# Optimization experiments

Hardware: AMD Instinct MI355X
Metric: run time of the kernel (lower is better)

The kernel has to match this reference:

```python
import jax, jax.numpy as jnp
import numpy as np

B, S, D = 1, 2048, 2048
H = 16            # num query heads
QL = 1536         # q_lora_rank
KVL = 512         # kv_lora_rank
DN = 128          # qk_nope_head_dim
DR = 64           # qk_rope_head_dim
DV = 128          # v_head_dim
F = 8192          # ffn intermediate
EPS = 1e-6
WAVE = 10000.0


def _rms(x, scale, eps=EPS):
    # fp32 norm then cast back, matching DeepSeekV3_1RMSNorm
    x32 = x.astype(jnp.float32)
    ms = jnp.mean(x32 * x32, axis=-1, keepdims=True)
    return (x32 * jax.lax.rsqrt(ms + eps)).astype(x.dtype) * scale


def _rope_tables(seq_len, dim):
    inv_freq = 1.0 / (WAVE ** (jnp.arange(0, dim, 2, dtype=jnp.float32) / dim))
    t = jnp.arange(seq_len, dtype=jnp.float32)[:, None] * inv_freq[None, :]  # [S, dim/2]
    emb = jnp.concatenate([t, t], axis=-1)  # [S, dim]
    return jnp.cos(emb), jnp.sin(emb)


def _apply_rope(x, cos, sin):
    # x: [B, S, H, dr]; rotate-half convention
    half = x.shape[-1] // 2
    x1, x2 = x[..., :half], x[..., half:]
    rot = jnp.concatenate([-x2, x1], axis=-1)
    return x * cos[None, :, None, :] + rot * sin[None, :, None, :]


def setup_inputs() -> dict:
    key = jax.random.key(0)
    ks = jax.random.split(key, 12)
    w = lambda k, shp: (jax.random.normal(k, shp, dtype=jnp.float32) * 0.02)
    inp = {
        "hidden_states": jax.random.normal(ks[0], (B, S, D), dtype=jnp.float32),
        "attention_mask": jnp.broadcast_to(jnp.tril(jnp.ones((S, S), dtype=bool)), (B, S, S)),
        "pre_attn_scale": jnp.ones((D,), jnp.float32),
        "wqa": w(ks[1], (D, QL)),
        "q_norm_scale": jnp.ones((QL,), jnp.float32),
        "wqb": w(ks[2], (QL, H * (DN + DR))),
        "wkva": w(ks[3], (D, KVL + DR)),
        "kv_norm_scale": jnp.ones((KVL,), jnp.float32),
        "wkvb": w(ks[4], (KVL, H * (DN + DV))),
        "wo": w(ks[5], (H * DV, D)),
        "pre_ffn_scale": jnp.ones((D,), jnp.float32),
        "wg": w(ks[6], (D, F)),
        "bg": jnp.zeros((F,), jnp.float32),
        "wu": w(ks[7], (D, F)),
        "bu": jnp.zeros((F,), jnp.float32),
        "wd": w(ks[8], (F, D)),
        "bd": jnp.zeros((D,), jnp.float32),
    }
    return inp


def reference(hidden_states, attention_mask, pre_attn_scale, wqa, q_norm_scale, wqb,
              wkva, kv_norm_scale, wkvb, wo, pre_ffn_scale, wg, bg, wu, bu, wd, bd):
    x = hidden_states
    # --- pre-attention RMSNorm ---
    n = _rms(x, pre_attn_scale)
    # --- MLA attention ---
    q = (_rms(n @ wqa, q_norm_scale) @ wqb).reshape(B, S, H, DN + DR)
    q_nope, q_rope = q[..., :DN], q[..., DN:]
    kva = n @ wkva                              # [B,S,KVL+DR]
    c_kv, k_rope = kva[..., :KVL], kva[..., KVL:]
    kv = (_rms(c_kv, kv_norm_scale) @ wkvb).reshape(B, S, H, DN + DV)
    k_nope, v = kv[..., :DN], kv[..., DN:]
    cos, sin = _rope_tables(S, DR)
    q_rope = _apply_rope(q_rope, cos, sin)
    k_rope = _apply_rope(k_rope[:, :, None, :], cos, sin)  # [B,S,1,DR] shared across heads
    qf = jnp.concatenate([q_nope, q_rope], axis=-1)
    kf = jnp.concatenate([k_nope, jnp.broadcast_to(k_rope, (B, S, H, DR))], axis=-1)
    scale = 1.0 / float(np.sqrt(DN + DR))
    scores = jnp.einsum('bqhd,bkhd->bhqk', qf, kf) * scale
    scores = jnp.where(attention_mask[:, None, :, :], scores, jnp.float32(-1e9))
    probs = jax.nn.softmax(scores, axis=-1)
    attn = jnp.einsum('bhqk,bkhd->bqhd', probs, v).reshape(B, S, H * DV)
    x = x + attn @ wo                            # residual 1 (dropout=0)
    # --- pre-FFN RMSNorm + dense SwiGLU FFN ---
    n = _rms(x, pre_ffn_scale)
    ff = (jax.nn.silu(n @ wg + bg) * (n @ wu + bu)) @ wd + bd
    return x + ff                                # residual 2
```

## Files before the change

kernel.cpp:

```cpp
#include <hip/hip_runtime.h>
#include <hip/hip_bf16.h>
#include <stdint.h>

typedef unsigned short u16;
using f32x4  = __attribute__((ext_vector_type(4))) float;
using bf16x8 = __attribute__((ext_vector_type(8))) __bf16;
using u32x4  = __attribute__((ext_vector_type(4))) uint32_t;
using u16x4  = __attribute__((ext_vector_type(4))) unsigned short;
using u16x8  = __attribute__((ext_vector_type(8))) unsigned short;

#define S_LEN 2048
#define DM    2048
#define NH    16
#define QLR   1536
#define KVLR  512
#define DNOPE 128
#define DROPE 64
#define DVAL  128
#define FFD   8192

static __device__ __forceinline__ float bf2f(u16 u) {
    union { uint32_t i; float f; } v; v.i = ((uint32_t)u) << 16; return v.f;
}
static __device__ __forceinline__ u16 f2bf(float f) {
    union { float f; uint32_t i; } v; v.f = f;
    uint32_t x = v.i;
    return (u16)((x + 0x7FFF + ((x >> 16) & 1)) >> 16);
}
static __device__ __forceinline__ void gload16(const u16* g, const u16* l) {
    __builtin_amdgcn_global_load_lds(
        (const __attribute__((address_space(1))) void*)g,
        (__attribute__((address_space(3))) void*)l, 16, 0, 0);
}

struct TWJob { const float* src; u16* dst; int R, C, xt, start; };
struct TWJobs { TWJob j[4]; };

__global__ __launch_bounds__(256)
void transpose_all(TWJobs jobs)
{
    __shared__ __align__(16) u16 tile[64][68];
    const int bid = blockIdx.x;
    int e = 0;
#pragma unroll
    for (int i = 1; i < 4; ++i) e = (bid >= jobs.j[i].start) ? i : e;
    const float* src = jobs.j[e].src;
    u16* dst = jobs.j[e].dst;
    const int R = jobs.j[e].R, C = jobs.j[e].C;
    const int local = bid - jobs.j[e].start;
    const int c0 = (local % jobs.j[e].xt) * 64;
    const int r0 = (local / jobs.j[e].xt) * 64;
    const int t = threadIdx.x;
#pragma unroll
    for (int i = 0; i < 4; ++i) {
        int idx = i * 256 + t;
        int r = idx >> 4, c4 = idx & 15;
        float4 v = *reinterpret_cast<const float4*>(&src[(size_t)(r0 + r) * C + c0 + c4 * 4]);
        u16x4 b; b[0] = f2bf(v.x); b[1] = f2bf(v.y); b[2] = f2bf(v.z); b[3] = f2bf(v.w);
        *reinterpret_cast<u16x4*>(&tile[r][c4 * 4]) = b;
    }
    __syncthreads();
#pragma unroll
    for (int i = 0; i < 4; ++i) {
        int idx = i * 256 + t;
        int rr = idx >> 4, k4 = idx & 15;
        u16x4 o;
#pragma unroll
        for (int j = 0; j < 4; ++j) o[j] = tile[k4 * 4 + j][rr];
        *reinterpret_cast<u16x4*>(&dst[(size_t)(c0 + rr) * R + r0 + k4 * 4]) = o;
    }
}

template<bool IN_F32>
__global__ __launch_bounds__(256)
void rms_norm(const void* __restrict__ in, int in_stride, int width,
              const float* __restrict__ scale, u16* __restrict__ out, int out_stride)
{
    const int row = blockIdx.x;
    const int t = threadIdx.x;
    const float* inf = (const float*)in;
    const u16*   inb = (const u16*)in;
    float ss = 0.f;
    for (int c = t; c < width; c += 256) {
        float v = IN_F32 ? inf[(size_t)row * in_stride + c] : bf2f(inb[(size_t)row * in_stride + c]);
        ss += v * v;
    }
#pragma unroll
    for (int o = 32; o > 0; o >>= 1) ss += __shfl_xor(ss, o);
    __shared__ float red[4];
    if ((t & 63) == 0) red[t >> 6] = ss;
    __syncthreads();
    float inv = rsqrtf((red[0] + red[1] + red[2] + red[3]) / (float)width + 1e-6f);
    for (int c = t; c < width; c += 256) {
        float v = IN_F32 ? inf[(size_t)row * in_stride + c] : bf2f(inb[(size_t)row * in_stride + c]);
        out[(size_t)row * out_stride + c] = f2bf(v * inv * scale[c]);
    }
}

__global__ __launch_bounds__(256)
void rms_norm2(const float* __restrict__ inA, int strideA, int widthA,
               const float* __restrict__ scaleA, u16* __restrict__ outA, int ostrA,
               const float* __restrict__ inB, int strideB, int widthB,
               const float* __restrict__ scaleB, u16* __restrict__ outB, int ostrB)
{
    const float* in   = blockIdx.y ? inB : inA;
    const float* scale= blockIdx.y ? scaleB : scaleA;
    u16* out          = blockIdx.y ? outB : outA;
    const int stride  = blockIdx.y ? strideB : strideA;
    const int width   = blockIdx.y ? widthB : widthA;
    const int ostr    = blockIdx.y ? ostrB : ostrA;
    const int row = blockIdx.x;
    const int t = threadIdx.x;
    float ss = 0.f;
    for (int c = t; c < width; c += 256) {
        float v = in[(size_t)row * stride + c];
        ss += v * v;
    }
#pragma unroll
    for (int o = 32; o > 0; o >>= 1) ss += __shfl_xor(ss, o);
    __shared__ float red[4];
    if ((t & 63) == 0) red[t >> 6] = ss;
    __syncthreads();
    float inv = rsqrtf((red[0] + red[1] + red[2] + red[3]) / (float)width + 1e-6f);
    for (int c = t; c < width; c += 256) {
        float v = in[(size_t)row * stride + c];
        out[(size_t)row * ostr + c] = f2bf(v * inv * scale[c]);
    }
}

__global__ __launch_bounds__(256)
void rope_tv(u16* __restrict__ q, const float* __restrict__ kva, u16* __restrict__ kr,
             const u16* __restrict__ kv, u16* __restrict__ vt)
{
    const int bid = blockIdx.x;
    const int t = threadIdx.x;
    if (bid < S_LEN) {
        const int s = bid;
        for (int idx = t; idx < 544; idx += 256) {
            int d = idx & 31;
            float invf = powf(10000.f, -(float)(2 * d) / 64.f);
            float ang = (float)s * invf;
            float cs = cosf(ang), sn = sinf(ang);
            if (idx < 512) {
                int hh = idx >> 5;
                u16* base = q + ((size_t)s * NH + hh) * 192 + 128;
                float x1 = bf2f(base[d]), x2 = bf2f(base[d + 32]);
                base[d]      = f2bf(x1 * cs - x2 * sn);
                base[d + 32] = f2bf(x2 * cs + x1 * sn);
            } else {
                const float* kb = kva + (size_t)s * 576 + 512;
                float x1 = kb[d], x2 = kb[d + 32];
                kr[(size_t)s * 64 + d]      = f2bf(x1 * cs - x2 * sn);
                kr[(size_t)s * 64 + d + 32] = f2bf(x2 * cs + x1 * sn);
            }
        }
        return;
    }
    __shared__ __align__(16) u16 tile[64][76];
    const int t2 = bid - S_LEN;
    const int s0 = (t2 & 31) * 64;
    const int d0 = ((t2 >> 5) & 1) * 64;
    const int h  = t2 >> 6;
#pragma unroll
    for (int i = 0; i < 2; ++i) {
        int idx = i * 256 + t;
        int s = idx >> 3, c8 = idx & 7;
        u16x8 v = *reinterpret_cast<const u16x8*>(kv + (size_t)(s0 + s) * (NH * 256) + h * 256 + 128 + d0 + c8 * 8);
        u16x4 lo, hi;
#pragma unroll
        for (int j = 0; j < 4; ++j) { lo[j] = v[j]; hi[j] = v[4 + j]; }
        *reinterpret_cast<u16x4*>(&tile[s][c8 * 8])     = lo;
        *reinterpret_cast<u16x4*>(&tile[s][c8 * 8 + 4]) = hi;
    }
    __syncthreads();
#pragma unroll
    for (int i = 0; i < 4; ++i) {
        int idx = i * 256 + t;
        int d = idx >> 4, s4 = idx & 15;
        u16x4 o;
#pragma unroll
        for (int j = 0; j < 4; ++j) o[j] = tile[s4 * 4 + j][d];
        *reinterpret_cast<u16x4*>(&vt[(size_t)(h * 128 + d0 + d) * S_LEN + s0 + s4 * 4]) = o;
    }
}

__global__ __launch_bounds__(256)
void init_out(const float* __restrict__ x2, const float* __restrict__ bd,
              float* __restrict__ out, int total4, int N)
{
    int i = blockIdx.x * 256 + threadIdx.x;
    const int stride = gridDim.x * 256;
    for (; i < total4; i += stride) {
        float4 r = ((const float4*)x2)[i];
        int col = (i * 4) & (N - 1);
        float4 b = *reinterpret_cast<const float4*>(&bd[col]);
        float4 o; o.x = r.x + b.x; o.y = r.y + b.y; o.z = r.z + b.z; o.w = r.w + b.w;
        ((float4*)out)[i] = o;
    }
}

__global__ __launch_bounds__(256)
void mul_gu(const u16* __restrict__ g, const u16* __restrict__ u,
            u16* __restrict__ h, int total8)
{
    int i = blockIdx.x * 256 + threadIdx.x;
    const int stride = gridDim.x * 256;
    for (; i < total8; i += stride) {
        u16x8 gv = ((const u16x8*)g)[i];
        u16x8 uv = ((const u16x8*)u)[i];
        u16x8 hv;
#pragma unroll
        for (int j = 0; j < 8; ++j) hv[j] = f2bf(bf2f(gv[j]) * bf2f(uv[j]));
        ((u16x8*)h)[i] = hv;
    }
}

struct GJob { const u16* A; const u16* BT; void* out; int N, K, yCount, zCount; };

template<int EPI>
__global__ __launch_bounds__(256)
void gemm_bt2(GJob j0, GJob j1)
{
    __shared__ __align__(16) u16 As[128 * 64];
    __shared__ __align__(16) u16 Bs[128 * 64];
    const int t = threadIdx.x;
    const int lane = t & 63;
    const int w = t >> 6;
    const int wr = w >> 1, wc = w & 1;
    const int li = lane & 15;
    const int lg = lane >> 4;

    const int gx = gridDim.x;
    int nwg = gx * gridDim.y;
    int bid = blockIdx.y * gx + blockIdx.x;
    bid = (bid & 7) * (nwg >> 3) + (bid >> 3);
    const int m0 = (bid % gx) * 128;
    int yy = bid / gx;

    const int j0span = j0.yCount * j0.zCount;
    const GJob& J = (yy < j0span) ? j0 : j1;
    if (yy >= j0span) yy -= j0span;
    const int ntile = yy % J.yCount;
    const int z = yy / J.yCount;
    const int n0 = ntile * 128;
    const int N = J.N, K = J.K;

    const int nktt = K >> 6;
    const int nz = J.zCount;
    const int qq = nktt / nz, rr = nktt % nz;
    const int kt0 = z * qq + (z < rr ? z : rr);
    const int ktEnd = kt0 + qq + (z < rr ? 1 : 0);

    const int srow = w * 32 + (lane >> 3);
    const int scol = (((lane & 7) ^ (lane >> 3)) << 3);
    const u16* ag = J.A  + (size_t)(m0 + srow) * K + scol;
    const u16* bg = J.BT + (size_t)(n0 + srow) * K + scol;

    f32x4 acc[4][4];
#pragma unroll
    for (int m = 0; m < 4; ++m)
#pragma unroll
        for (int n = 0; n < 4; ++n)
            acc[m][n] = f32x4{0.f, 0.f, 0.f, 0.f};

    for (int kt = kt0; kt < ktEnd; ++kt) {
        const int k0 = kt << 6;
        __syncthreads();
#pragma unroll
        for (int i = 0; i < 4; ++i) {
            gload16(ag + (size_t)i * 8 * K + k0, As + (w * 32 + i * 8) * 64);
            gload16(bg + (size_t)i * 8 * K + k0, Bs + (w * 32 + i * 8) * 64);
        }
        __syncthreads();
#pragma unroll
        for (int kk = 0; kk < 2; ++kk) {
            const int csw = (kk * 32 + lg * 8) ^ ((li & 7) << 3);
            bf16x8 af[4], bfr[4];
#pragma unroll
            for (int m = 0; m < 4; ++m)
                af[m] = *reinterpret_cast<const bf16x8*>(As + (wr * 64 + m * 16 + li) * 64 + csw);
#pragma unroll
            for (int n = 0; n < 4; ++n)
                bfr[n] = *reinterpret_cast<const bf16x8*>(Bs + (wc * 64 + n * 16 + li) * 64 + csw);
#pragma unroll
            for (int m = 0; m < 4; ++m)
#pragma unroll
                for (int n = 0; n < 4; ++n)
                    acc[m][n] = __builtin_amdgcn_mfma_f32_16x16x32_bf16(af[m], bfr[n], acc[m][n], 0, 0, 0);
        }
    }

#pragma unroll
    for (int m = 0; m < 4; ++m) {
        const int row = m0 + wr * 64 + m * 16 + lg * 4;
#pragma unroll
        for (int n = 0; n < 4; ++n) {
            const int col = n0 + wc * 64 + n * 16 + li;
            if (col < N) {
#pragma unroll
                for (int r2 = 0; r2 < 4; ++r2) {
                    float v = acc[m][n][r2];
                    size_t idx = (size_t)(row + r2) * N + col;
                    if (EPI == 0) ((u16*)J.out)[idx] = f2bf(v);
                    else          unsafeAtomicAdd((float*)J.out + idx, v);
                }
            }
        }
    }
}

struct BJob { const u16* A; const u16* BT; u16* out; int N, K, yCount; };

__global__ __launch_bounds__(512, 4)
void gemm_big2(BJob j0, BJob j1)
{
    __shared__ __align__(16) u16 As[256 * 64];
    __shared__ __align__(16) u16 Bs[128 * 64];
    const int t = threadIdx.x;
    const int lane = t & 63;
    const int w = t >> 6;
    const int wr = w >> 1, wc = w & 1;
    const int li = lane & 15;
    const int lg = lane >> 4;

    const int gx = gridDim.x;
    int nwg = gx * gridDim.y;
    int bid = blockIdx.y * gx + blockIdx.x;
    bid = (bid & 7) * (nwg >> 3) + (bid >> 3);
    const int m0 = (bid % gx) * 256;
    int yy = bid / gx;

    const BJob& J = (yy < j0.yCount) ? j0 : j1;
    if (yy >= j0.yCount) yy -= j0.yCount;
    const int n0 = yy * 128;
    const int N = J.N, K = J.K;

    const int sr = lane >> 3;
    const int scol = (((lane & 7) ^ sr) << 3);
    const u16* ag = J.A  + (size_t)(m0 + w * 8 + sr) * K + scol;
    const u16* bg = J.BT + (size_t)(n0 + w * 8 + sr) * K + scol;
    const u16* lA = As + (w * 8) * 64;
    const u16* lB = Bs + (w * 8) * 64;

    f32x4 acc[4][4];
#pragma unroll
    for (int m = 0; m < 4; ++m)
#pragma unroll
        for (int n = 0; n < 4; ++n)
            acc[m][n] = f32x4{0.f, 0.f, 0.f, 0.f};

    const int nkt = K >> 6;
    for (int kt = 0; kt < nkt; ++kt) {
        const int k0 = kt << 6;
        __syncthreads();
#pragma unroll
        for (int i = 0; i < 4; ++i)
            gload16(ag + (size_t)i * 64 * K + k0, lA + i * 64 * 64);
#pragma unroll
        for (int i = 0; i < 2; ++i)
            gload16(bg + (size_t)i * 64 * K + k0, lB + i * 64 * 64);
        __syncthreads();
        __builtin_amdgcn_s_setprio(1);
#pragma unroll
        for (int kk = 0; kk < 2; ++kk) {
            const int csw = (kk * 32 + lg * 8) ^ ((li & 7) << 3);
            bf16x8 af[4], bfr[4];
#pragma unroll
            for (int m = 0; m < 4; ++m)
                af[m] = *reinterpret_cast<const bf16x8*>(As + (wr * 64 + m * 16 + li) * 64 + csw);
#pragma unroll
            for (int n = 0; n < 4; ++n)
                bfr[n] = *reinterpret_cast<const bf16x8*>(Bs + (wc * 64 + n * 16 + li) * 64 + csw);
#pragma unroll
            for (int m = 0; m < 4; ++m)
#pragma unroll
                for (int n = 0; n < 4; ++n)
                    acc[m][n] = __builtin_amdgcn_mfma_f32_16x16x32_bf16(af[m], bfr[n], acc[m][n], 0, 0, 0);
        }
        __builtin_amdgcn_s_setprio(0);
    }

#pragma unroll
    for (int m = 0; m < 4; ++m) {
        const int row = m0 + wr * 64 + m * 16 + lg * 4;
#pragma unroll
        for (int n = 0; n < 4; ++n) {
            const int col = n0 + wc * 64 + n * 16 + li;
#pragma unroll
            for (int r2 = 0; r2 < 4; ++r2)
                J.out[(size_t)(row + r2) * N + col] = f2bf(acc[m][n][r2]);
        }
    }
}

template<int EPI>
__global__ __launch_bounds__(512, 4)
void gemm_big(const u16* __restrict__ A, const u16* __restrict__ BT,
              void* __restrict__ out, int M, int N, int K,
              const float* __restrict__ bias, const u16* __restrict__ gmul)
{
    __shared__ __align__(16) u16 As[256 * 64];
    __shared__ __align__(16) u16 Bs[128 * 64];
    const int t = threadIdx.x;
    const int lane = t & 63;
    const int w = t >> 6;
    const int wr = w >> 1, wc = w & 1;
    const int li = lane & 15;
    const int lg = lane >> 4;

    const int gx = gridDim.x;
    int nwg = gx * gridDim.y;
    int bid = blockIdx.y * gx + blockIdx.x;
    bid = (bid & 7) * (nwg >> 3) + (bid >> 3);
    const int m0 = (bid % gx) * 256;
    const int n0 = (bid / gx) * 128;

    const int nz = gridDim.z, z = blockIdx.z;
    const int nktt = K >> 6;
    const int qq = nktt / nz, rr = nktt % nz;
    const int kt0 = z * qq + (z < rr ? z : rr);
    const int ktEnd = kt0 + qq + (z < rr ? 1 : 0);

    const int sr = lane >> 3;
    const int scol = (((lane & 7) ^ sr) << 3);
    const u16* ag = A  + (size_t)(m0 + w * 8 + sr) * K + scol;
    const u16* bg = BT + (size_t)(n0 + w * 8 + sr) * K + scol;
    const u16* lA = As + (w * 8) * 64;
    const u16* lB = Bs + (w * 8) * 64;

    f32x4 acc[4][4];
#pragma unroll
    for (int m = 0; m < 4; ++m)
#pragma unroll
        for (int n = 0; n < 4; ++n)
            acc[m][n] = f32x4{0.f, 0.f, 0.f, 0.f};

    for (int kt = kt0; kt < ktEnd; ++kt) {
        const int k0 = kt << 6;
        __syncthreads();
#pragma unroll
        for (int i = 0; i < 4; ++i)
            gload16(ag + (size_t)i * 64 * K + k0, lA + i * 64 * 64);
#pragma unroll
        for (int i = 0; i < 2; ++i)
            gload16(bg + (size_t)i * 64 * K + k0, lB + i * 64 * 64);
        __syncthreads();
        __builtin_amdgcn_s_setprio(1);
#pragma unroll
        for (int kk = 0; kk < 2; ++kk) {
            const int csw = (kk * 32 + lg * 8) ^ ((li & 7) << 3);
            bf16x8 af[4], bfr[4];
#pragma unroll
            for (int m = 0; m < 4; ++m)
                af[m] = *reinterpret_cast<const bf16x8*>(As + (wr * 64 + m * 16 + li) * 64 + csw);
#pragma unroll
            for (int n = 0; n < 4; ++n)
                bfr[n] = *reinterpret_cast<const bf16x8*>(Bs + (wc * 64 + n * 16 + li) * 64 + csw);
#pragma unroll
            for (int m = 0; m < 4; ++m)
#pragma unroll
                for (int n = 0; n < 4; ++n)
                    acc[m][n] = __builtin_amdgcn_mfma_f32_16x16x32_bf16(af[m], bfr[n], acc[m][n], 0, 0, 0);
        }
        __builtin_amdgcn_s_setprio(0);
    }

#pragma unroll
    for (int m = 0; m < 4; ++m) {
        const int row = m0 + wr * 64 + m * 16 + lg * 4;
#pragma unroll
        for (int n = 0; n < 4; ++n) {
            const int col = n0 + wc * 64 + n * 16 + li;
#pragma unroll
            for (int r2 = 0; r2 < 4; ++r2) {
                float v = acc[m][n][r2];
                size_t idx = (size_t)(row + r2) * N + col;
                if (EPI == 0) ((u16*)out)[idx] = f2bf(v);
                else          unsafeAtomicAdd((float*)out + idx, v);
            }
        }
    }
}

__global__ __launch_bounds__(512, 4)
void gemm_gu(const u16* __restrict__ A, const u16* __restrict__ BgT, const u16* __restrict__ BuT,
             u16* __restrict__ gout, u16* __restrict__ uout, int M, int N, int K,
             const float* __restrict__ bg, const float* __restrict__ bu)
{
    __shared__ __align__(16) u16 As[256 * 64];
    __shared__ __align__(16) u16 Bs[128 * 64];
    const int t = threadIdx.x;
    const int lane = t & 63;
    const int w = t >> 6;
    const int wr = w >> 1, wc = w & 1;
    const int li = lane & 15;
    const int lg = lane >> 4;
    const int isUp = blockIdx.z;

    const u16* BT = isUp ? BuT : BgT;
    const float* bias = isUp ? bu : bg;
    u16* out = isUp ? uout : gout;

    const int gx = gridDim.x;
    int nwg = gx * gridDim.y;
    int bid = blockIdx.y * gx + blockIdx.x;
    bid = (bid & 7) * (nwg >> 3) + (bid >> 3);
    const int m0 = (bid % gx) * 256;
    const int n0 = (bid / gx) * 128;

    const int sr = lane >> 3;
    const int scol = (((lane & 7) ^ sr) << 3);
    const u16* ag = A  + (size_t)(m0 + w * 8 + sr) * K + scol;
    const u16* bgp = BT + (size_t)(n0 + w * 8 + sr) * K + scol;
    const u16* lA = As + (w * 8) * 64;
    const u16* lB = Bs + (w * 8) * 64;

    f32x4 acc[4][4];
#pragma unroll
    for (int m = 0; m < 4; ++m)
#pragma unroll
        for (int n = 0; n < 4; ++n)
            acc[m][n] = f32x4{0.f, 0.f, 0.f, 0.f};

    const int nkt = K >> 6;
    for (int kt = 0; kt < nkt; ++kt) {
        const int k0 = kt << 6;
        __syncthreads();
#pragma unroll
        for (int i = 0; i < 4; ++i)
            gload16(ag + (size_t)i * 64 * K + k0, lA + i * 64 * 64);
#pragma unroll
        for (int i = 0; i < 2; ++i)
            gload16(bgp + (size_t)i * 64 * K + k0, lB + i * 64 * 64);
        __syncthreads();
        __builtin_amdgcn_s_setprio(1);
#pragma unroll
        for (int kk = 0; kk < 2; ++kk) {
            const int csw = (kk * 32 + lg * 8) ^ ((li & 7) << 3);
            bf16x8 af[4], bfr[4];
#pragma unroll
            for (int m = 0; m < 4; ++m)
                af[m] = *reinterpret_cast<const bf16x8*>(As + (wr * 64 + m * 16 + li) * 64 + csw);
#pragma unroll
            for (int n = 0; n < 4; ++n)
                bfr[n] = *reinterpret_cast<const bf16x8*>(Bs + (wc * 64 + n * 16 + li) * 64 + csw);
#pragma unroll
            for (int m = 0; m < 4; ++m)
#pragma unroll
                for (int n = 0; n < 4; ++n)
                    acc[m][n] = __builtin_amdgcn_mfma_f32_16x16x32_bf16(af[m], bfr[n], acc[m][n], 0, 0, 0);
        }
        __builtin_amdgcn_s_setprio(0);
    }

#pragma unroll
    for (int m = 0; m < 4; ++m) {
        const int row = m0 + wr * 64 + m * 16 + lg * 4;
#pragma unroll
        for (int n = 0; n < 4; ++n) {
            const int col = n0 + wc * 64 + n * 16 + li;
            float bv = bias[col];
#pragma unroll
            for (int r2 = 0; r2 < 4; ++r2) {
                float v = acc[m][n][r2] + bv;
                if (!isUp) v = v / (1.f + __expf(-v));
                out[(size_t)(row + r2) * N + col] = f2bf(v);
            }
        }
    }
}

struct TW4 { const float* src; u16* dst; int R, C, xt, gstart; };
struct TW4s { TW4 j[4]; };

__global__ __launch_bounds__(512)
void attn_tw(const u16* __restrict__ q, const u16* __restrict__ kv,
             const u16* __restrict__ kr, const u16* __restrict__ vt,
             u16* __restrict__ attn, TW4s tj)
{
    __shared__ __align__(16) u16 SMEM[2 * 20480 + 8 * 16 * 72];

    if (blockIdx.y >= 16) {
        u16 (*tile)[68] = reinterpret_cast<u16(*)[68]>(SMEM);
        const int g = (blockIdx.y - 16) * 16 + blockIdx.x;
        int e = 0;
#pragma unroll
        for (int i = 1; i < 4; ++i) e = (g >= tj.j[i].gstart) ? i : e;
        const float* src = tj.j[e].src;
        u16* dst = tj.j[e].dst;
        const int R = tj.j[e].R, C = tj.j[e].C, xt = tj.j[e].xt;
        const int base = (g - tj.j[e].gstart) * 8;
        const int t = threadIdx.x;
        for (int ti = 0; ti < 8; ++ti) {
            const int local = base + ti;
            const int c0 = (local % xt) * 64;
            const int r0 = (local / xt) * 64;
            __syncthreads();
#pragma unroll
            for (int i = 0; i < 2; ++i) {
                int idx = i * 512 + t;
                int r = idx >> 4, c4 = idx & 15;
                float4 v = *reinterpret_cast<const float4*>(&src[(size_t)(r0 + r) * C + c0 + c4 * 4]);
                u16x4 b; b[0] = f2bf(v.x); b[1] = f2bf(v.y); b[2] = f2bf(v.z); b[3] = f2bf(v.w);
                *reinterpret_cast<u16x4*>(&tile[r][c4 * 4]) = b;
            }
            __syncthreads();
#pragma unroll
            for (int i = 0; i < 2; ++i) {
                int idx = i * 512 + t;
                int rr = idx >> 4, k4 = idx & 15;
                u16x4 o;
#pragma unroll
                for (int j = 0; j < 4; ++j) o[j] = tile[k4 * 4 + j][rr];
                *reinterpret_cast<u16x4*>(&dst[(size_t)(c0 + rr) * R + r0 + k4 * 4]) = o;
            }
        }
        return;
    }

    u16 (*KVs)[20480] = reinterpret_cast<u16(*)[20480]>(SMEM);
    u16 (*Ps)[16][72] = reinterpret_cast<u16(*)[16][72]>(SMEM + 2 * 20480);

    const int t = threadIdx.x;
    const int lane = t & 63;
    const int w = t >> 6;
    const int li = lane & 15;
    const int lg = lane >> 4;
    const int h = blockIdx.x;
    const int b = 15 - blockIdx.y;

    const int qt = (w < 4) ? (2 * b + 1) : (2 * b);
    const int my_nkt = qt + 1;
    const int block_nkt = 2 * b + 2;
    const int wl = w & 3;
    const int qr = qt * 64 + wl * 16;
    const int qpos = qr + li;

    auto stage = [&](int buf, int k0) {
        u16* base = &KVs[buf][0];
#pragma unroll
        for (int i = 0; i < 3; ++i) {
            int g = w * 3 + i;
            int P = g * 64 + lane;
            int j = P / 24, s = P % 24;
            int c = (s & 24) | ((s ^ (j & 7)) & 7);
            const u16* src = (c < 16)
                ? kv + (size_t)(k0 + j) * (NH * 256) + h * 256 + c * 8
                : kr + (size_t)(k0 + j) * 64 + (c - 16) * 8;
            gload16(src, base + g * 512);
        }
#pragma unroll
        for (int i = 0; i < 2; ++i) {
            int g = w * 2 + i;
            int P = g * 64 + lane;
            int d = P >> 3, s8 = P & 7;
            int c = s8 ^ (d & 7);
            const u16* src = vt + (size_t)(h * 128 + d) * S_LEN + k0 + c * 8;
            gload16(src, base + 12288 + g * 512);
        }
    };

    bf16x8 qf[6];
#pragma unroll
    for (int kb = 0; kb < 6; ++kb)
        qf[kb] = *reinterpret_cast<const bf16x8*>(q + ((size_t)(qr + li) * NH + h) * 192 + kb * 32 + lg * 8);

    f32x4 oacc[8];
#pragma unroll
    for (int i = 0; i < 8; ++i) oacc[i] = f32x4{0.f, 0.f, 0.f, 0.f};
    float m_run = -INFINITY, l_run = 0.f;

    stage(0, 0);
    int buf = 0;
    const float scale = 0.07216878364870322f;

    for (int kt = 0; kt < block_nkt; ++kt) {
        const int k0 = kt << 6;
        __syncthreads();
        if (kt + 1 < block_nkt) stage(buf ^ 1, (kt + 1) << 6);

        if (kt < my_nkt) {
            const u16* bb = &KVs[buf][0];

            f32x4 sacc[4];
#pragma unroll
            for (int jt = 0; jt < 4; ++jt) sacc[jt] = f32x4{0.f, 0.f, 0.f, 0.f};
            __builtin_amdgcn_s_setprio(1);
#pragma unroll
            for (int kb = 0; kb < 6; ++kb) {
                const int c = kb * 4 + lg;
                const int s = (c & 24) | ((c ^ (li & 7)) & 7);
#pragma unroll
                for (int jt = 0; jt < 4; ++jt) {
                    bf16x8 kf = *reinterpret_cast<const bf16x8*>(bb + ((jt * 16 + li) * 24 + s) * 8);
                    sacc[jt] = __builtin_amdgcn_mfma_f32_16x16x32_bf16(kf, qf[kb], sacc[jt], 0, 0, 0);
                }
            }
            __builtin_amdgcn_s_setprio(0);

            float p[16];
            float mt = -INFINITY;
            if (k0 + 63 <= qr) {
#pragma unroll
                for (int jt = 0; jt < 4; ++jt)
#pragma unroll
                    for (int r = 0; r < 4; ++r) {
                        float sv = sacc[jt][r] * scale;
                        p[jt * 4 + r] = sv;
                        mt = fmaxf(mt, sv);
                    }
            } else {
#pragma unroll
                for (int jt = 0; jt < 4; ++jt)
#pragma unroll
                    for (int r = 0; r < 4; ++r) {
                        int jpos = k0 + jt * 16 + lg * 4 + r;
                        float sv = (jpos <= qpos) ? sacc[jt][r] * scale : -INFINITY;
                        p[jt * 4 + r] = sv;
                        mt = fmaxf(mt, sv);
                    }
            }
            mt = fmaxf(mt, __shfl_xor(mt, 16));
            mt = fmaxf(mt, __shfl_xor(mt, 32));
            if (!__all(mt <= m_run + 8.f)) {
                float mn = fmaxf(m_run, mt);
                float sf = __expf(m_run - mn);
                float sfr[4];
#pragma unroll
                for (int r = 0; r < 4; ++r)
                    sfr[r] = __shfl(sf, (lane & 48) + lg * 4 + r);
#pragma unroll
                for (int d2 = 0; d2 < 8; ++d2)
#pragma unroll
                    for (int r = 0; r < 4; ++r)
                        oacc[d2][r] *= sfr[r];
                l_run *= sf;
                m_run = mn;
            }
            float rsum = 0.f;
#pragma unroll
            for (int i2 = 0; i2 < 16; ++i2) { p[i2] = __expf(p[i2] - m_run); rsum += p[i2]; }
            rsum += __shfl_xor(rsum, 16);
            rsum += __shfl_xor(rsum, 32);
            l_run += rsum;

#pragma unroll
            for (int jt = 0; jt < 4; ++jt) {
                u16x4 pk;
                pk[0] = f2bf(p[jt * 4 + 0]); pk[1] = f2bf(p[jt * 4 + 1]);
                pk[2] = f2bf(p[jt * 4 + 2]); pk[3] = f2bf(p[jt * 4 + 3]);
                *reinterpret_cast<u16x4*>(&Ps[w][li][jt * 16 + lg * 4]) = pk;
            }

            __builtin_amdgcn_s_setprio(1);
#pragma unroll
            for (int ks = 0; ks < 2; ++ks) {
                bf16x8 pf = *reinterpret_cast<const bf16x8*>(&Ps[w][li][ks * 32 + lg * 8]);
                const int vs = (ks * 4 + lg) ^ (li & 7);
#pragma unroll
                for (int d2 = 0; d2 < 8; ++d2) {
                    bf16x8 vf = *reinterpret_cast<const bf16x8*>(bb + 12288 + ((d2 * 16 + li) * 8 + vs) * 8);
                    oacc[d2] = __builtin_amdgcn_mfma_f32_16x16x32_bf16(pf, vf, oacc[d2], 0, 0, 0);
                }
            }
            __builtin_amdgcn_s_setprio(0);
        }
        buf ^= 1;
    }

    float rl = 1.f / l_run;
    float rlr[4];
#pragma unroll
    for (int r = 0; r < 4; ++r)
        rlr[r] = __shfl(rl, (lane & 48) + lg * 4 + r);
#pragma unroll
    for (int d2 = 0; d2 < 8; ++d2)
#pragma unroll
        for (int r = 0; r < 4; ++r) {
            int srow = qr + lg * 4 + r;
            int dcol = d2 * 16 + li;
            attn[(size_t)srow * (NH * DVAL) + h * DVAL + dcol] = f2bf(oacc[d2][r] * rlr[r]);
        }
}

extern "C" void kernel_launch(void* const* d_in, const int* in_sizes, int n_in,
                              void* d_out, int out_size, void* d_ws, size_t ws_size,
                              hipStream_t stream)
{
    const float* hidden   = (const float*)d_in[0];
    const float* pa_scale = (const float*)d_in[2];
    const float* wqa      = (const float*)d_in[3];
    const float* qn_scale = (const float*)d_in[4];
    const float* wqb      = (const float*)d_in[5];
    const float* wkva     = (const float*)d_in[6];
    const float* kv_scale = (const float*)d_in[7];
    const float* wkvb     = (const float*)d_in[8];
    const float* wo       = (const float*)d_in[9];
    const float* pf_scale = (const float*)d_in[10];
    const float* wg       = (const float*)d_in[11];
    const float* bg       = (const float*)d_in[12];
    const float* wu       = (const float*)d_in[13];
    const float* bu       = (const float*)d_in[14];
    const float* wd       = (const float*)d_in[15];
    const float* bd       = (const float*)d_in[16];
    float* out = (float*)d_out;

    size_t off = 0;
    auto alloc = [&](size_t bytes) {
        off = (off + 255) & ~(size_t)255;
        void* p = (char*)d_ws + off;
        off += bytes;
        return p;
    };
    u16* wqaT  = (u16*)alloc((size_t)QLR * DM * 2);
    u16* wqbT  = (u16*)alloc((size_t)3072 * QLR * 2);
    u16* wkvaT = (u16*)alloc((size_t)640 * DM * 2);
    u16* wkvbT = (u16*)alloc((size_t)4096 * KVLR * 2);
    u16* woT   = (u16*)alloc((size_t)DM * DM * 2);
    u16* wgT   = (u16*)alloc((size_t)FFD * DM * 2);
    u16* wuT   = (u16*)alloc((size_t)FFD * DM * 2);
    u16* wdT   = (u16*)alloc((size_t)DM * FFD * 2);
    u16* n1    = (u16*)alloc((size_t)S_LEN * DM * 2);
    float* qlora32 = (float*)alloc((size_t)S_LEN * QLR * 4);
    float* kva32   = (float*)alloc((size_t)S_LEN * 576 * 4);
    u16* qn    = (u16*)alloc((size_t)S_LEN * QLR * 2);
    u16* qbuf  = (u16*)alloc((size_t)S_LEN * 3072 * 2);
    u16* ckvn  = (u16*)alloc((size_t)S_LEN * KVLR * 2);
    u16* kvbuf = (u16*)alloc((size_t)S_LEN * 4096 * 2);
    u16* krbuf = (u16*)alloc((size_t)S_LEN * 64 * 2);
    u16* attnb = (u16*)alloc((size_t)S_LEN * DM * 2);
    float* x2  = (float*)alloc((size_t)S_LEN * DM * 4);
    u16* n2    = (u16*)alloc((size_t)S_LEN * DM * 2);
    u16* gbuf  = (u16*)alloc((size_t)S_LEN * FFD * 2);
    u16* hbuf  = (u16*)alloc((size_t)S_LEN * FFD * 2);
    u16* vtb  = (u16*)qlora32;
    u16* ubuf = (u16*)qlora32;
    (void)ws_size; (void)in_sizes; (void)n_in; (void)out_size;

    TWJobs ejobs;
    int startAcc = 0;
    auto setE = [&](int i, const float* s, u16* d, int R, int C) {
        ejobs.j[i] = TWJob{s, d, R, C, C / 64, startAcc};
        startAcc += (C / 64) * (R / 64);
    };
    setE(0, wqa,  wqaT,  2048, 1536);
    setE(1, wqb,  wqbT,  1536, 3072);
    setE(2, wkva, wkvaT, 2048,  576);
    setE(3, wkvb, wkvbT,  512, 4096);
    hipLaunchKernelGGL(transpose_all, dim3(startAcc), 256, 0, stream, ejobs);

    hipMemsetAsync(qlora32, 0, (size_t)S_LEN * QLR * 4, stream);
    hipMemsetAsync(kva32,   0, (size_t)S_LEN * 576 * 4, stream);

    hipLaunchKernelGGL((rms_norm<true>),  dim3(S_LEN), 256, 0, stream, hidden, DM, DM, pa_scale, n1, DM);

    {
        GJob jqa  {n1, wqaT,  qlora32, QLR, DM, 12, 2};
        GJob jkva {n1, wkvaT, kva32,   576, DM,  5, 4};
        hipLaunchKernelGGL((gemm_bt2<5>), dim3(16, 44), 256, 0, stream, jqa, jkva);
    }
    hipLaunchKernelGGL(rms_norm2, dim3(S_LEN, 2), 256, 0, stream,
                       qlora32, QLR, QLR, qn_scale, qn, QLR,
                       kva32, 576, KVLR, kv_scale, ckvn, KVLR);
    {
        BJob jqb  {qn,   wqbT,  qbuf,  3072, QLR,  24};
        BJob jkvb {ckvn, wkvbT, kvbuf, 4096, KVLR, 32};
        hipLaunchKernelGGL(gemm_big2, dim3(8, 56), 512, 0, stream, jqb, jkvb);
    }
    hipLaunchKernelGGL(rope_tv, dim3(S_LEN + 1024), 256, 0, stream, qbuf, kva32, krbuf, kvbuf, vtb);

    TW4s tj;
    int gAcc = 0;
    auto setL = [&](int i, const float* s, u16* d, int R, int C) {
        tj.j[i] = TW4{s, d, R, C, C / 64, gAcc};
        gAcc += (C / 64) * (R / 64) / 8;
    };
    setL(0, wo, woT, 2048, 2048);
    setL(1, wg, wgT, 2048, 8192);
    setL(2, wu, wuT, 2048, 8192);
    setL(3, wd, wdT, 8192, 2048);
    hipLaunchKernelGGL(attn_tw, dim3(16, 16 + 104), 512, 0, stream, qbuf, kvbuf, krbuf, vtb, attnb, tj);

    hipMemcpyAsync(x2, hidden, (size_t)S_LEN * DM * 4, hipMemcpyDeviceToDevice, stream);
    hipLaunchKernelGGL((gemm_big<5>), dim3(8, 16, 4), 512, 0, stream, attnb, woT, x2, S_LEN, DM, DM, nullptr, nullptr);

    hipLaunchKernelGGL((rms_norm<true>), dim3(S_LEN), 256, 0, stream, x2, DM, DM, pf_scale, n2, DM);

    hipLaunchKernelGGL(init_out, dim3(2048), 256, 0, stream, x2, bd, out, S_LEN * DM / 4, DM);
    hipLaunchKernelGGL(gemm_gu, dim3(8, 64, 2), 512, 0, stream, n2, wgT, wuT, gbuf, ubuf, S_LEN, FFD, DM, bg, bu);
    hipLaunchKernelGGL(mul_gu, dim3(2048), 256, 0, stream, gbuf, ubuf, hbuf, S_LEN * FFD / 8);
    hipLaunchKernelGGL((gemm_big<5>), dim3(8, 16, 4), 512, 0, stream, hbuf, wdT, out, S_LEN, DM, FFD, nullptr, nullptr);
}
```

Baseline: 597.7 us.

## Fuse residual copy, bias init and gate-up multiply into neighboring kernels

```diff
diff --git a/kernel.cpp b/kernel.cpp
--- a/kernel.cpp
+++ b/kernel.cpp
@@ -71,18 +71,16 @@
     }
 }
 
-template<bool IN_F32>
 __global__ __launch_bounds__(256)
-void rms_norm(const void* __restrict__ in, int in_stride, int width,
-              const float* __restrict__ scale, u16* __restrict__ out, int out_stride)
+void rms_norm_copy(const float* __restrict__ in, int width,
+                   const float* __restrict__ scale, u16* __restrict__ out,
+                   float* __restrict__ copy_out)
 {
     const int row = blockIdx.x;
     const int t = threadIdx.x;
-    const float* inf = (const float*)in;
-    const u16*   inb = (const u16*)in;
     float ss = 0.f;
     for (int c = t; c < width; c += 256) {
-        float v = IN_F32 ? inf[(size_t)row * in_stride + c] : bf2f(inb[(size_t)row * in_stride + c]);
+        float v = in[(size_t)row * width + c];
         ss += v * v;
     }
 #pragma unroll
@@ -92,8 +90,34 @@
     __syncthreads();
     float inv = rsqrtf((red[0] + red[1] + red[2] + red[3]) / (float)width + 1e-6f);
     for (int c = t; c < width; c += 256) {
-        float v = IN_F32 ? inf[(size_t)row * in_stride + c] : bf2f(inb[(size_t)row * in_stride + c]);
-        out[(size_t)row * out_stride + c] = f2bf(v * inv * scale[c]);
+        float v = in[(size_t)row * width + c];
+        out[(size_t)row * width + c] = f2bf(v * inv * scale[c]);
+        copy_out[(size_t)row * width + c] = v;
+    }
+}
+
+__global__ __launch_bounds__(256)
+void rms_norm_bias(const float* __restrict__ in, int width,
+                   const float* __restrict__ scale, u16* __restrict__ out,
+                   const float* __restrict__ bd, float* __restrict__ outf)
+{
+    const int row = blockIdx.x;
+    const int t = threadIdx.x;
+    float ss = 0.f;
+    for (int c = t; c < width; c += 256) {
+        float v = in[(size_t)row * width + c];
+        ss += v * v;
+    }
+#pragma unroll
+    for (int o = 32; o > 0; o >>= 1) ss += __shfl_xor(ss, o);
+    __shared__ float red[4];
+    if ((t & 63) == 0) red[t >> 6] = ss;
+    __syncthreads();
+    float inv = rsqrtf((red[0] + red[1] + red[2] + red[3]) / (float)width + 1e-6f);
+    for (int c = t; c < width; c += 256) {
+        float v = in[(size_t)row * width + c];
+        out[(size_t)row * width + c] = f2bf(v * inv * scale[c]);
+        outf[(size_t)row * width + c] = v + bd[c];
     }
 }
 
@@ -184,37 +208,6 @@
     }
 }
 
-__global__ __launch_bounds__(256)
-void init_out(const float* __restrict__ x2, const float* __restrict__ bd,
-              float* __restrict__ out, int total4, int N)
-{
-    int i = blockIdx.x * 256 + threadIdx.x;
-    const int stride = gridDim.x * 256;
-    for (; i < total4; i += stride) {
-        float4 r = ((const float4*)x2)[i];
-        int col = (i * 4) & (N - 1);
-        float4 b = *reinterpret_cast<const float4*>(&bd[col]);
-        float4 o; o.x = r.x + b.x; o.y = r.y + b.y; o.z = r.z + b.z; o.w = r.w + b.w;
-        ((float4*)out)[i] = o;
-    }
-}
-
-__global__ __launch_bounds__(256)
-void mul_gu(const u16* __restrict__ g, const u16* __restrict__ u,
-            u16* __restrict__ h, int total8)
-{
-    int i = blockIdx.x * 256 + threadIdx.x;
-    const int stride = gridDim.x * 256;
-    for (; i < total8; i += stride) {
-        u16x8 gv = ((const u16x8*)g)[i];
-        u16x8 uv = ((const u16x8*)u)[i];
-        u16x8 hv;
-#pragma unroll
-        for (int j = 0; j < 8; ++j) hv[j] = f2bf(bf2f(gv[j]) * bf2f(uv[j]));
-        ((u16x8*)h)[i] = hv;
-    }
-}
-
 struct GJob { const u16* A; const u16* BT; void* out; int N, K, yCount, zCount; };
 
 template<int EPI>
@@ -478,6 +471,101 @@
                 if (EPI == 0) ((u16*)out)[idx] = f2bf(v);
                 else          unsafeAtomicAdd((float*)out + idx, v);
             }
+        }
+    }
+}
+
+__global__ __launch_bounds__(512, 4)
+void gemm_wd(const u16* __restrict__ G, const u16* __restrict__ U,
+             const u16* __restrict__ BT, float* __restrict__ out,
+             int M, int N, int K)
+{
+    __shared__ __align__(16) u16 As[256 * 64];
+    __shared__ __align__(16) u16 Bs[128 * 64];
+    const int t = threadIdx.x;
+    const int lane = t & 63;
+    const int w = t >> 6;
+    const int wr = w >> 1, wc = w & 1;
+    const int li = lane & 15;
+    const int lg = lane >> 4;
+
+    const int gx = gridDim.x;
+    int nwg = gx * gridDim.y;
+    int bid = blockIdx.y * gx + blockIdx.x;
+    bid = (bid & 7) * (nwg >> 3) + (bid >> 3);
+    const int m0 = (bid % gx) * 256;
+    const int n0 = (bid / gx) * 128;
+
+    const int nz = gridDim.z, z = blockIdx.z;
+    const int nktt = K >> 6;
+    const int qq = nktt / nz, rr = nktt % nz;
+    const int kt0 = z * qq + (z < rr ? z : rr);
+    const int ktEnd = kt0 + qq + (z < rr ? 1 : 0);
+
+    const int sr = lane >> 3;
+    const int scol = (((lane & 7) ^ sr) << 3);
+    const u16* gg = G  + (size_t)(m0 + w * 8 + sr) * K + scol;
+    const u16* ug = U  + (size_t)(m0 + w * 8 + sr) * K + scol;
+    const u16* bg = BT + (size_t)(n0 + w * 8 + sr) * K + scol;
+    u16* lA = As + (w * 8) * 64;
+    const u16* lB = Bs + (w * 8) * 64;
+
+    f32x4 acc[4][4];
+#pragma unroll
+    for (int m = 0; m < 4; ++m)
+#pragma unroll
+        for (int n = 0; n < 4; ++n)
+            acc[m][n] = f32x4{0.f, 0.f, 0.f, 0.f};
+
+    for (int kt = kt0; kt < ktEnd; ++kt) {
+        const int k0 = kt << 6;
+        __syncthreads();
+#pragma unroll
+        for (int i = 0; i < 2; ++i)
+            gload16(bg + (size_t)i * 64 * K + k0, lB + i * 64 * 64);
+        u16x8 gr[4], ur[4];
+#pragma unroll
+        for (int i = 0; i < 4; ++i) {
+            gr[i] = *reinterpret_cast<const u16x8*>(gg + (size_t)i * 64 * K + k0);
+            ur[i] = *reinterpret_cast<const u16x8*>(ug + (size_t)i * 64 * K + k0);
+        }
+#pragma unroll
+        for (int i = 0; i < 4; ++i) {
+            u16x8 hv;
+#pragma unroll
+            for (int j = 0; j < 8; ++j) hv[j] = f2bf(bf2f(gr[i][j]) * bf2f(ur[i][j]));
+            *reinterpret_cast<u16x8*>(lA + i * 64 * 64 + lane * 8) = hv;
+        }
+        __syncthreads();
+        __builtin_amdgcn_s_setprio(1);
+#pragma unroll
+        for (int kk = 0; kk < 2; ++kk) {
+            const int csw = (kk * 32 + lg * 8) ^ ((li & 7) << 3);
+            bf16x8 af[4], bfr[4];
+#pragma unroll
+            for (int m = 0; m < 4; ++m)
+                af[m] = *reinterpret_cast<const bf16x8*>(As + (wr * 64 + m * 16 + li) * 64 + csw);
+#pragma unroll
+            for (int n = 0; n < 4; ++n)
+                bfr[n] = *reinterpret_cast<const bf16x8*>(Bs + (wc * 64 + n * 16 + li) * 64 + csw);
+#pragma unroll
+            for (int m = 0; m < 4; ++m)
+#pragma unroll
+                for (int n = 0; n < 4; ++n)
+                    acc[m][n] = __builtin_amdgcn_mfma_f32_16x16x32_bf16(af[m], bfr[n], acc[m][n], 0, 0, 0);
+        }
+        __builtin_amdgcn_s_setprio(0);
+    }
+
+#pragma unroll
+    for (int m = 0; m < 4; ++m) {
+        const int row = m0 + wr * 64 + m * 16 + lg * 4;
+#pragma unroll
+        for (int n = 0; n < 4; ++n) {
+            const int col = n0 + wc * 64 + n * 16 + li;
+#pragma unroll
+            for (int r2 = 0; r2 < 4; ++r2)
+                unsafeAtomicAdd(out + (size_t)(row + r2) * N + col, acc[m][n][r2]);
         }
     }
 }
@@ -835,7 +923,7 @@
     u16* hbuf  = (u16*)alloc((size_t)S_LEN * FFD * 2);
     u16* vtb  = (u16*)qlora32;
     u16* ubuf = (u16*)qlora32;
-    (void)ws_size; (void)in_sizes; (void)n_in; (void)out_size;
+    (void)ws_size; (void)in_sizes; (void)n_in; (void)out_size; (void)hbuf;
 
     TWJobs ejobs;
     int startAcc = 0;
@@ -852,7 +940,7 @@
     hipMemsetAsync(qlora32, 0, (size_t)S_LEN * QLR * 4, stream);
     hipMemsetAsync(kva32,   0, (size_t)S_LEN * 576 * 4, stream);
 
-    hipLaunchKernelGGL((rms_norm<true>),  dim3(S_LEN), 256, 0, stream, hidden, DM, DM, pa_scale, n1, DM);
+    hipLaunchKernelGGL(rms_norm_copy, dim3(S_LEN), 256, 0, stream, hidden, DM, pa_scale, n1, x2);
 
     {
         GJob jqa  {n1, wqaT,  qlora32, QLR, DM, 12, 2};
@@ -881,13 +969,10 @@
     setL(3, wd, wdT, 8192, 2048);
     hipLaunchKernelGGL(attn_tw, dim3(16, 16 + 104), 512, 0, stream, qbuf, kvbuf, krbuf, vtb, attnb, tj);
 
-    hipMemcpyAsync(x2, hidden, (size_t)S_LEN * DM * 4, hipMemcpyDeviceToDevice, stream);
     hipLaunchKernelGGL((gemm_big<5>), dim3(8, 16, 4), 512, 0, stream, attnb, woT, x2, S_LEN, DM, DM, nullptr, nullptr);
 
-    hipLaunchKernelGGL((rms_norm<true>), dim3(S_LEN), 256, 0, stream, x2, DM, DM, pf_scale, n2, DM);
-
-    hipLaunchKernelGGL(init_out, dim3(2048), 256, 0, stream, x2, bd, out, S_LEN * DM / 4, DM);
+    hipLaunchKernelGGL(rms_norm_bias, dim3(S_LEN), 256, 0, stream, x2, DM, pf_scale, n2, bd, out);
+
     hipLaunchKernelGGL(gemm_gu, dim3(8, 64, 2), 512, 0, stream, n2, wgT, wuT, gbuf, ubuf, S_LEN, FFD, DM, bg, bu);
-    hipLaunchKernelGGL(mul_gu, dim3(2048), 256, 0, stream, gbuf, ubuf, hbuf, S_LEN * FFD / 8);
-    hipLaunchKernelGGL((gemm_big<5>), dim3(8, 16, 4), 512, 0, stream, hbuf, wdT, out, S_LEN, DM, FFD, nullptr, nullptr);
-}
+    hipLaunchKernelGGL(gemm_wd, dim3(8, 16, 4), 512, 0, stream, gbuf, ubuf, wdT, out, S_LEN, DM, FFD);
+}
```

Result: no change. 607.9 us (+1.7%).
